# Performance work log

Hardware: AMD Instinct MI355X
Metric: run time of the kernel (lower is better)

Reference implementation:

```python
import jax, jax.numpy as jnp
import numpy as np

jax.config.update("jax_enable_x64", True)

N = 16          # particles per jet
B = 32          # number of jets
L2 = 1e-4       # qpth_l2_strength ('L2' form: Q = L2*I, p = flattened distance matrix)
ITERS = 20      # fixed interior-point iterations (converges well past solver tolerance)
SIGMA = 0.1     # centering parameter


def _build_G(n):
    # Inequality matrix, same layout as the torch code: G = [-I ; marginal-row-sums ; marginal-col-sums]
    m = n * n
    G1 = -np.eye(m)
    G2 = np.zeros((2 * n, m))
    for i in range(n):
        G2[i, i * n:(i + 1) * n] = 1.0      # sum_j x_{ij} <= w1_i
    for j in range(n):
        G2[n + j, j::n] = 1.0               # sum_i x_{ij} <= w2_j
    return jnp.asarray(np.concatenate([G1, G2], axis=0))  # [m + 2n, m]


def _solve_qp(p, h, b, G):
    """Batched infeasible-start primal-dual interior point solver for
    min 0.5*L2*||x||^2 + p.x  s.t.  G x <= h,  1.x = b  (same QP qpth solves)."""
    Bn, m = p.shape
    nin = G.shape[0]
    ones_m = jnp.ones((m,), p.dtype)
    x = jnp.zeros((Bn, m), p.dtype)
    s = jnp.ones((Bn, nin), p.dtype)
    z = jnp.ones((Bn, nin), p.dtype)
    y = jnp.zeros((Bn,), p.dtype)
    eye_m = jnp.eye(m, dtype=p.dtype)

    def step(carry, _):
        x, s, z, y = carry
        mu = jnp.mean(s * z, axis=1)                    # [B]
        rx = L2 * x + p + z @ G + y[:, None]            # dual residual   (A^T y = y * 1)
        rp = x @ G.T + s - h                            # primal ineq residual
        ra = x.sum(1) - b                               # primal eq residual
        rs = s * z - SIGMA * mu[:, None]                # complementarity residual
        d = z / s
        # H = Q + G^T diag(d) G  -> [B, m, m]
        H = L2 * eye_m + jnp.einsum('rk,br,rl->bkl', G, d, G)
        r1 = rx + ((z * rp - rs) / s) @ G
        Lc = jnp.linalg.cholesky(H)

        def chosolve(rhs):  # rhs [B, m] -> H^{-1} rhs
            t = jax.scipy.linalg.solve_triangular(Lc, rhs[..., None], lower=True)
            return jax.scipy.linalg.solve_triangular(Lc, t, lower=True, trans='T')[..., 0]

        u = chosolve(r1)
        v = chosolve(jnp.broadcast_to(ones_m, (Bn, m)))
        dy = (ra - u.sum(1)) / v.sum(1)                 # Schur complement on the 1-row equality
        dx = -u - v * dy[:, None]
        ds = -rp - dx @ G.T
        dz = (-rs - z * ds) / s
        # fraction-to-boundary step
        ds_safe = jnp.where(ds < 0, ds, -jnp.ones_like(ds))
        dz_safe = jnp.where(dz < 0, dz, -jnp.ones_like(dz))
        a_s = jnp.min(jnp.where(ds < 0, -s / ds_safe, jnp.inf), axis=1)
        a_z = jnp.min(jnp.where(dz < 0, -z / dz_safe, jnp.inf), axis=1)
        alpha = 0.99 * jnp.minimum(1.0, jnp.minimum(a_s, a_z))[:, None]
        x = x + alpha * dx
        s = s + alpha * ds
        z = z + alpha * dz
        y = y + alpha[:, 0] * dy
        return (x, s, z, y), None

    (x, s, z, y), _ = jax.lax.scan(step, (x, s, z, y), None, length=ITERS)
    return x


def setup_inputs() -> dict:
    key = jax.random.key(0)
    k1, k2 = jax.random.split(key)
    jets1 = jax.random.uniform(k1, (B, N, 3), dtype=jnp.float32)
    jets2 = jax.random.uniform(k2, (B, N, 3), dtype=jnp.float32)
    return {"jets1": jets1, "jets2": jets2}


def reference(jets1, jets2):
    j1 = jets1.astype(jnp.float64)
    j2 = jets2.astype(jnp.float64)
    nb, n = j1.shape[0], j1.shape[1]
    # pairwise (eta, phi) distances, same sign/epsilon as the torch code
    diffs = -(j1[:, :, None, :2] - j2[:, None, :, :2]) + 1e-12   # [B, n, n, 2]
    dists = jnp.sqrt(jnp.sum(diffs * diffs, axis=3))             # [B, n, n]
    w1 = j1[:, :, 2]
    w2 = j2[:, :, 2]
    p = dists.reshape(nb, n * n)
    h = jnp.concatenate([jnp.zeros((nb, n * n), p.dtype), w1, w2], axis=1)
    b = jnp.minimum(w1.sum(1), w2.sum(1))
    G = _build_G(n)
    flow = _solve_qp(p, h, b, G)                                  # [B, n*n]
    energy_diff = jnp.abs(w1.sum(1) - w2.sum(1))
    emds = jnp.sum(p * flow, axis=1) + energy_diff                # [B]
    return emds
```

## Files before the change

kernel.cpp:

```cpp
#include <hip/hip_runtime.h>
#include <math.h>

#define L2C  1e-4
#define SIGC 0.1
#define NITER 20

#if defined(__has_builtin)
#  if __has_builtin(__builtin_amdgcn_permlane16_swap) && __has_builtin(__builtin_amdgcn_permlane32_swap)
#    define HAVE_PLSWAP 1
#  endif
#  if __has_builtin(__builtin_amdgcn_rcp)
#    define HAVE_RCP64 1
#  endif
#endif
#ifndef HAVE_PLSWAP
#  define HAVE_PLSWAP 0
#endif
#ifndef HAVE_RCP64
#  define HAVE_RCP64 0
#endif

__device__ __forceinline__ double rld(double v, int lane) {
    union { double d; int i[2]; } u, r; u.d = v;
    r.i[0] = __builtin_amdgcn_readlane(u.i[0], lane);
    r.i[1] = __builtin_amdgcn_readlane(u.i[1], lane);
    return r.d;
}
template <int CTRL>
__device__ __forceinline__ double dppd(double v) {
    union { double d; int i[2]; } u, r; u.d = v;
    r.i[0] = __builtin_amdgcn_update_dpp(0, u.i[0], CTRL, 0xF, 0xF, true);
    r.i[1] = __builtin_amdgcn_update_dpp(0, u.i[1], CTRL, 0xF, 0xF, true);
    return r.d;
}
__device__ __forceinline__ double sum16d(double v) {
    v += dppd<0xB1>(v); v += dppd<0x4E>(v); v += dppd<0x124>(v); v += dppd<0x128>(v);
    return v;
}
template <int CTRL>
__device__ __forceinline__ float dppf(float v) {
    return __int_as_float(__builtin_amdgcn_update_dpp(0, __float_as_int(v), CTRL, 0xF, 0xF, true));
}
__device__ __forceinline__ float min16f(float v) {
    v = fminf(v, dppf<0xB1>(v)); v = fminf(v, dppf<0x4E>(v));
    v = fminf(v, dppf<0x124>(v)); v = fminf(v, dppf<0x128>(v));
    return v;
}
__device__ __forceinline__ double mkd(unsigned lo, unsigned hi) {
    union { unsigned u[2]; double d; } r; r.u[0] = lo; r.u[1] = hi; return r.d;
}
__device__ __forceinline__ void dsplit(double v, unsigned &lo, unsigned &hi) {
    union { double d; unsigned u[2]; } x; x.d = v; lo = x.u[0]; hi = x.u[1];
}
__device__ __forceinline__ double cross4d(double v) {
#if HAVE_PLSWAP
    unsigned lo, hi; dsplit(v, lo, hi);
    auto rl = __builtin_amdgcn_permlane16_swap(lo, lo, false, false);
    auto rh = __builtin_amdgcn_permlane16_swap(hi, hi, false, false);
    v = mkd(rl[0], rh[0]) + mkd(rl[1], rh[1]);
    dsplit(v, lo, hi);
    auto sl = __builtin_amdgcn_permlane32_swap(lo, lo, false, false);
    auto sh = __builtin_amdgcn_permlane32_swap(hi, hi, false, false);
    return mkd(sl[0], sh[0]) + mkd(sl[1], sh[1]);
#else
    v += __shfl_xor(v, 16, 64); v += __shfl_xor(v, 32, 64); return v;
#endif
}
__device__ __forceinline__ float cross4minf(float v) {
#if HAVE_PLSWAP
    auto a = __builtin_amdgcn_permlane16_swap(__float_as_uint(v), __float_as_uint(v), false, false);
    v = fminf(__uint_as_float(a[0]), __uint_as_float(a[1]));
    auto b = __builtin_amdgcn_permlane32_swap(__float_as_uint(v), __float_as_uint(v), false, false);
    return fminf(__uint_as_float(b[0]), __uint_as_float(b[1]));
#else
    v = fminf(v, __shfl_xor(v, 16, 64)); v = fminf(v, __shfl_xor(v, 32, 64)); return v;
#endif
}
__device__ __forceinline__ double drcp(double d) {
#if HAVE_RCP64
    double x = __builtin_amdgcn_rcp(d);
#else
    double x = (double)__builtin_amdgcn_rcpf((float)d);
#endif
    x = x * (2.0 - d * x);
    return x;
}
__device__ __forceinline__ float frcpf(float x) { return __builtin_amdgcn_rcpf(x); }

__global__ __launch_bounds__(64, 1) void emd_ip_kernel(const float* __restrict__ jets1,
                                                       const float* __restrict__ jets2,
                                                       float* __restrict__ out) {
    const int l = threadIdx.x;
    const int b = blockIdx.x;
    const int q = l & 15;
    const int r = l >> 4;

    __shared__ double invDl[16 * 17];
    __shared__ double Sst[16 * 17];
    __shared__ double Lst[16 * 17];
    __shared__ double GstR[16], GstI[16];

    const float* p1 = jets1 + b * 48;
    const float* p2 = jets2 + b * 48;

    double ax = (double)p1[3 * q], ay = (double)p1[3 * q + 1];
    double px[4];
#pragma unroll
    for (int c = 0; c < 4; c++) {
        int j = 4 * c + r;
        double d0 = ((double)p2[3 * j]     - ax) + 1e-12;
        double d1 = ((double)p2[3 * j + 1] - ay) + 1e-12;
        px[c] = sqrt(d0 * d0 + d1 * d1);
    }
    double h_rt = (double)p1[3 * q + 2];
    double h_ct[4];
#pragma unroll
    for (int c = 0; c < 4; c++) h_ct[c] = (double)p2[3 * (4 * c + r) + 2];

    double sw1 = sum16d(h_rt);
    double sw2 = sum16d((double)p2[3 * q + 2]);
    const double sB = fmin(sw1, sw2);
    const double sE = fabs(sw1 - sw2);

    double x[4] = {0, 0, 0, 0}, s[4] = {1, 1, 1, 1}, z[4] = {1, 1, 1, 1};
    double yv = 0.0;
    double s_rt = 1.0, z_rt = 1.0;
    double s_ct[4] = {1, 1, 1, 1}, z_ct[4] = {1, 1, 1, 1};
    double rsx = 0.0;
    double cs[4] = {0, 0, 0, 0};
    double ra = -sB;

    for (int it = 0; it < NITER; ++it) {
        double is_rt = drcp(s_rt);
        double iz_rt = drcp(z_rt);
        double srz   = s_rt * iz_rt;
        double is_ct[4], iz_ct[4];
#pragma unroll
        for (int c = 0; c < 4; c++) { is_ct[c] = drcp(s_ct[c]); iz_ct[c] = drcp(z_ct[c]); }
        double is_[4], iD[4];
#pragma unroll
        for (int c = 0; c < 4; c++) {
            is_[c] = drcp(s[c]);
            iD[c] = drcp(L2C + z[c] * is_[c]);
            invDl[q * 17 + 4 * c + r] = iD[c];
        }

        double mub = s[0]*z[0] + s[1]*z[1] + s[2]*z[2] + s[3]*z[3]
                   + 0.25 * (s_rt * z_rt)
                   + 0.0625 * (s_ct[0]*z_ct[0] + s_ct[1]*z_ct[1] + s_ct[2]*z_ct[2] + s_ct[3]*z_ct[3]);
        double mu = sum16d(cross4d(mub)) * (1.0 / 288.0);
        if (!(mu >= 1e-4)) break;
        double sgmu = SIGC * mu;

        double rp_rt = rsx + s_rt - h_rt;
        double rs_rt = s_rt * z_rt - sgmu;
        double tt_rt = (z_rt * (rsx - h_rt) + sgmu) * is_rt;
        double rp_ct[4], rs_ct[4], tt_ct[4];
#pragma unroll
        for (int c = 0; c < 4; c++) {
            rp_ct[c] = cs[c] + s_ct[c] - h_ct[c];
            rs_ct[c] = s_ct[c] * z_ct[c] - sgmu;
            tt_ct[c] = (z_ct[c] * (cs[c] - h_ct[c]) + sgmu) * is_ct[c];
        }

        double rp[4], rs[4], r1[4], rD1[4];
#pragma unroll
        for (int c = 0; c < 4; c++) {
            double rx = L2C * x[c] + px[c] + (-z[c] + z_rt + z_ct[c]) + yv;
            rp[c] = s[c] - x[c];
            rs[c] = s[c] * z[c] - sgmu;
            double tk = (sgmu - z[c] * x[c]) * is_[c];
            r1[c] = rx - tk + tt_rt + tt_ct[c];
            rD1[c] = r1[c] * iD[c];
        }

        double rsI = cross4d(iD[0] + iD[1] + iD[2] + iD[3]);
        double rsR = cross4d(rD1[0] + rD1[1] + rD1[2] + rD1[3]);
        double csI[4], csR[4];
#pragma unroll
        for (int c = 0; c < 4; c++) { csI[c] = sum16d(iD[c]); csR[c] = sum16d(rD1[c]); }

        double ar = drcp(srz + rsI);
        double aR = ar * rsR;
        double aI = ar * rsI;

        double gpR[4], gpI[4], bb[4];
#pragma unroll
        for (int c = 0; c < 4; c++) {
            gpR[c] = csR[c] - sum16d(aR * iD[c]);
            gpI[c] = csI[c] - sum16d(aI * iD[c]);
            bb[c]  = s_ct[c] * iz_ct[c] + csI[c];
            if (q == 4 * c + r) { GstR[q] = gpR[c]; GstI[q] = gpI[c]; }
        }

        double accA[4] = {0, 0, 0, 0}, accB[4] = {0, 0, 0, 0};
#pragma unroll
        for (int t = 0; t < 8; t++) {
            double wA = rld(ar, t) * invDl[t * 17 + q];
            double wB = rld(ar, t + 8) * invDl[(t + 8) * 17 + q];
#pragma unroll
            for (int c = 0; c < 4; c++) {
                accA[c] += wA * invDl[t * 17 + 4 * c + r];
                accB[c] += wB * invDl[(t + 8) * 17 + 4 * c + r];
            }
        }
#pragma unroll
        for (int c = 0; c < 4; c++)
            Sst[q * 17 + 4 * c + r] = ((q == 4 * c + r) ? bb[c] : 0.0) - (accA[c] + accB[c]);

        double Sr[16];
#pragma unroll
        for (int j2 = 0; j2 < 16; j2++) Sr[j2] = Sst[q * 17 + j2];

        double flo[16];
#pragma unroll
        for (int kk = 0; kk < 16; kk++)
            flo[kk] = fmax(1e-12 * fabs(rld(Sr[kk], kk)), 1e-280);

        double invdv = 0.0;
        double pcand = 0.0;
#pragma unroll
        for (int kk = 0; kk < 16; kk++) {
            double praw = (kk == 0) ? rld(Sr[0], 0) : rld(pcand, kk);
            double dkk = fmax(praw, flo[kk]);
            double inv = drcp(dkk);
            invdv = (q == kk) ? inv : invdv;
            double Lc = Sr[kk] * inv;
            if (l < 16) Lst[kk * 17 + l] = Lc;
            if (kk < 15) pcand = Sr[kk + 1] - Sr[kk] * Lc;
#pragma unroll
            for (int jj = kk + 1; jj < 16; jj++)
                Sr[jj] -= Sr[kk] * rld(Lc, jj);
            Sr[kk] = Lc;
        }

        double y1 = GstR[q], y2 = GstI[q];
        double LTr[16];
#pragma unroll
        for (int kk = 0; kk < 16; kk++) LTr[kk] = Lst[q * 17 + kk];

#pragma unroll
        for (int kk = 0; kk < 16; kk++) {
            double t1 = rld(y1, kk);
            double t2 = rld(y2, kk);
            if (q > kk) { y1 -= Sr[kk] * t1; y2 -= Sr[kk] * t2; }
        }
        y1 *= invdv;
        y2 *= invdv;
#pragma unroll
        for (int kk = 15; kk >= 0; kk--) {
            double t1 = rld(y1, kk);
            double t2 = rld(y2, kk);
            if (q < kk) { y1 -= LTr[kk] * t1; y2 -= LTr[kk] * t2; }
        }

        double qc1c[4], qcvc[4];
#pragma unroll
        for (int c = 0; c < 4; c++) {
            qc1c[c] = __shfl(y1, 4 * c + r, 64);
            qcvc[c] = __shfl(y2, 4 * c + r, 64);
        }

        double pr1 = iD[0]*qc1c[0] + iD[1]*qc1c[1] + iD[2]*qc1c[2] + iD[3]*qc1c[3];
        double prv = iD[0]*qcvc[0] + iD[1]*qcvc[1] + iD[2]*qcvc[2] + iD[3]*qcvc[3];
        double qr1 = ar * (rsR - cross4d(pr1));
        double qrv = ar * (rsI - cross4d(prv));

        double u[4], v[4];
#pragma unroll
        for (int c = 0; c < 4; c++) {
            u[c] = (r1[c] - qr1 - qc1c[c]) * iD[c];
            v[c] = (1.0  - qrv - qcvc[c]) * iD[c];
        }
        double usum = sum16d(cross4d(u[0] + u[1] + u[2] + u[3]));
        double vsum = sum16d(cross4d(v[0] + v[1] + v[2] + v[3]));
        double dy = (ra - usum) * drcp(vsum);

        double dx[4];
#pragma unroll
        for (int c = 0; c < 4; c++) dx[c] = -u[c] - v[c] * dy;
        double rsdx = cross4d(dx[0] + dx[1] + dx[2] + dx[3]);
        double csdx[4];
#pragma unroll
        for (int c = 0; c < 4; c++) csdx[c] = sum16d(dx[c]);
        double sumdx = -usum - vsum * dy;

        float amP = 1e30f, amD = 1e30f;
        double ds[4], dz[4];
#pragma unroll
        for (int c = 0; c < 4; c++) {
            ds[c] = dx[c] - rp[c];
            dz[c] = -(rs[c] + z[c] * ds[c]) * is_[c];
            if (ds[c] < 0.0) amP = fminf(amP, (float)s[c] * frcpf((float)(-ds[c])));
            if (dz[c] < 0.0) amD = fminf(amD, (float)z[c] * frcpf((float)(-dz[c])));
        }
        double ds_rt = -rp_rt - rsdx;
        double dz_rt = -(rs_rt + z_rt * ds_rt) * is_rt;
        if (ds_rt < 0.0) amP = fminf(amP, (float)s_rt * frcpf((float)(-ds_rt)));
        if (dz_rt < 0.0) amD = fminf(amD, (float)z_rt * frcpf((float)(-dz_rt)));
        double ds_ct[4], dz_ct[4];
#pragma unroll
        for (int c = 0; c < 4; c++) {
            ds_ct[c] = -rp_ct[c] - csdx[c];
            dz_ct[c] = -(rs_ct[c] + z_ct[c] * ds_ct[c]) * is_ct[c];
            if (ds_ct[c] < 0.0) amP = fminf(amP, (float)s_ct[c] * frcpf((float)(-ds_ct[c])));
            if (dz_ct[c] < 0.0) amD = fminf(amD, (float)z_ct[c] * frcpf((float)(-dz_ct[c])));
        }
        float aPf = min16f(cross4minf(amP));
        float aDf = min16f(cross4minf(amD));
        double alphaP = 0.99 * fmin(1.0, (double)aPf);
        double alphaD = 0.99 * fmin(1.0, (double)aDf);
        bool good = ((dy - dy) == 0.0);
        alphaP = good ? alphaP : 0.0;
        alphaD = good ? alphaD : 0.0;

#pragma unroll
        for (int c = 0; c < 4; c++) {
            x[c] += alphaP * dx[c];
            s[c] += alphaP * ds[c];
            z[c] += alphaD * dz[c];
            s_ct[c] += alphaP * ds_ct[c];
            z_ct[c] += alphaD * dz_ct[c];
            cs[c] += alphaP * csdx[c];
        }
        yv += alphaD * dy;
        s_rt += alphaP * ds_rt;
        z_rt += alphaD * dz_rt;
        rsx += alphaP * rsdx;
        ra  += alphaP * sumdx;
    }

    double e = sum16d(cross4d(px[0]*x[0] + px[1]*x[1] + px[2]*x[2] + px[3]*x[3]));
    if (l == 0) out[b] = (float)(e + sE);
}

extern "C" void kernel_launch(void* const* d_in, const int* in_sizes, int n_in,
                              void* d_out, int out_size, void* d_ws, size_t ws_size,
                              hipStream_t stream) {
    const float* jets1 = (const float*)d_in[0];
    const float* jets2 = (const float*)d_in[1];
    float* out = (float*)d_out;
    int B = in_sizes[0] / 48;
    emd_ip_kernel<<<dim3(B), dim3(64), 0, stream>>>(jets1, jets2, out);
}
```

Measured before the change: 113.0 us.

## Share reciprocals, fuse forward solve into Cholesky, transpose Schur matrix via permlane swaps

Each pair of reciprocals, such as 1/s and 1/z, is now computed from a single reciprocal of their product. The Schur matrix is transposed with permlane16/32 swaps instead of a round trip through LDS, guarded by a runtime check of the swap semantics. The two right-hand sides are packed into one register split across half-waves, and the forward substitution is folded into the Cholesky factorization loop. A few reductions are merged, and rsdx is derived algebraically. Together these cut readlane, LDS and reciprocal work on the serial per-iteration critical path, at some risk to rounding behaviour and to correctness of the permlane assumptions.

```diff
diff --git a/kernel.cpp b/kernel.cpp
--- a/kernel.cpp
+++ b/kernel.cpp
@@ -98,7 +98,7 @@
     __shared__ double invDl[16 * 17];
     __shared__ double Sst[16 * 17];
     __shared__ double Lst[16 * 17];
-    __shared__ double GstR[16], GstI[16];
+    __shared__ double Gst[2][16];
 
     const float* p1 = jets1 + b * 48;
     const float* p2 = jets2 + b * 48;
@@ -122,6 +122,17 @@
     const double sB = fmin(sw1, sw2);
     const double sE = fabs(sw1 - sw2);
 
+#if HAVE_PLSWAP
+    auto pr16 = __builtin_amdgcn_permlane16_swap((unsigned)l, (unsigned)l, false, false);
+    auto pr32 = __builtin_amdgcn_permlane32_swap((unsigned)l, (unsigned)l, false, false);
+    const bool convOK = (__builtin_amdgcn_readfirstlane((int)pr16[0]) == 0) &&
+                        (__builtin_amdgcn_readfirstlane((int)pr16[1]) == 16) &&
+                        (__builtin_amdgcn_readfirstlane((int)pr32[0]) == 0) &&
+                        (__builtin_amdgcn_readfirstlane((int)pr32[1]) == 32);
+#else
+    const bool convOK = false;
+#endif
+
     double x[4] = {0, 0, 0, 0}, s[4] = {1, 1, 1, 1}, z[4] = {1, 1, 1, 1};
     double yv = 0.0;
     double s_rt = 1.0, z_rt = 1.0;
@@ -131,35 +142,44 @@
     double ra = -sB;
 
     for (int it = 0; it < NITER; ++it) {
-        double is_rt = drcp(s_rt);
-        double iz_rt = drcp(z_rt);
-        double srz   = s_rt * iz_rt;
-        double is_ct[4], iz_ct[4];
-#pragma unroll
-        for (int c = 0; c < 4; c++) { is_ct[c] = drcp(s_ct[c]); iz_ct[c] = drcp(z_ct[c]); }
-        double is_[4], iD[4];
-#pragma unroll
-        for (int c = 0; c < 4; c++) {
-            is_[c] = drcp(s[c]);
-            iD[c] = drcp(L2C + z[c] * is_[c]);
+        double prt = s_rt * z_rt;
+        double irt = drcp(prt);
+        double is_rt = z_rt * irt, iz_rt = s_rt * irt;
+        double srz = (s_rt * s_rt) * irt;
+        double pct[4], is_ct[4], iz_ct[4];
+#pragma unroll
+        for (int c = 0; c < 4; c++) {
+            pct[c] = s_ct[c] * z_ct[c];
+            double ict = drcp(pct[c]);
+            is_ct[c] = z_ct[c] * ict;
+            iz_ct[c] = s_ct[c] * ict;
+        }
+        double szc[4], is_[4], iD[4];
+#pragma unroll
+        for (int c = 0; c < 4; c++) {
+            szc[c] = s[c] * z[c];
+            double tc = fma(L2C, s[c], z[c]);
+            double ip = drcp(s[c] * tc);
+            is_[c] = tc * ip;
+            iD[c]  = (s[c] * s[c]) * ip;
             invDl[q * 17 + 4 * c + r] = iD[c];
         }
 
-        double mub = s[0]*z[0] + s[1]*z[1] + s[2]*z[2] + s[3]*z[3]
-                   + 0.25 * (s_rt * z_rt)
-                   + 0.0625 * (s_ct[0]*z_ct[0] + s_ct[1]*z_ct[1] + s_ct[2]*z_ct[2] + s_ct[3]*z_ct[3]);
+        double mub = szc[0] + szc[1] + szc[2] + szc[3]
+                   + 0.25 * prt
+                   + 0.0625 * (pct[0] + pct[1] + pct[2] + pct[3]);
         double mu = sum16d(cross4d(mub)) * (1.0 / 288.0);
         if (!(mu >= 1e-4)) break;
         double sgmu = SIGC * mu;
 
         double rp_rt = rsx + s_rt - h_rt;
-        double rs_rt = s_rt * z_rt - sgmu;
+        double rs_rt = prt - sgmu;
         double tt_rt = (z_rt * (rsx - h_rt) + sgmu) * is_rt;
         double rp_ct[4], rs_ct[4], tt_ct[4];
 #pragma unroll
         for (int c = 0; c < 4; c++) {
             rp_ct[c] = cs[c] + s_ct[c] - h_ct[c];
-            rs_ct[c] = s_ct[c] * z_ct[c] - sgmu;
+            rs_ct[c] = pct[c] - sgmu;
             tt_ct[c] = (z_ct[c] * (cs[c] - h_ct[c]) + sgmu) * is_ct[c];
         }
 
@@ -168,7 +188,7 @@
         for (int c = 0; c < 4; c++) {
             double rx = L2C * x[c] + px[c] + (-z[c] + z_rt + z_ct[c]) + yv;
             rp[c] = s[c] - x[c];
-            rs[c] = s[c] * z[c] - sgmu;
+            rs[c] = szc[c] - sgmu;
             double tk = (sgmu - z[c] * x[c]) * is_[c];
             r1[c] = rx - tk + tt_rt + tt_ct[c];
             rD1[c] = r1[c] * iD[c];
@@ -176,21 +196,21 @@
 
         double rsI = cross4d(iD[0] + iD[1] + iD[2] + iD[3]);
         double rsR = cross4d(rD1[0] + rD1[1] + rD1[2] + rD1[3]);
-        double csI[4], csR[4];
-#pragma unroll
-        for (int c = 0; c < 4; c++) { csI[c] = sum16d(iD[c]); csR[c] = sum16d(rD1[c]); }
+        double csI[4];
+#pragma unroll
+        for (int c = 0; c < 4; c++) csI[c] = sum16d(iD[c]);
 
         double ar = drcp(srz + rsI);
         double aR = ar * rsR;
         double aI = ar * rsI;
 
-        double gpR[4], gpI[4], bb[4];
-#pragma unroll
-        for (int c = 0; c < 4; c++) {
-            gpR[c] = csR[c] - sum16d(aR * iD[c]);
-            gpI[c] = csI[c] - sum16d(aI * iD[c]);
-            bb[c]  = s_ct[c] * iz_ct[c] + csI[c];
-            if (q == 4 * c + r) { GstR[q] = gpR[c]; GstI[q] = gpI[c]; }
+        double bb[4];
+#pragma unroll
+        for (int c = 0; c < 4; c++) {
+            double gpR = sum16d(rD1[c] - aR * iD[c]);
+            double gpI = csI[c] - sum16d(aI * iD[c]);
+            bb[c] = s_ct[c] * iz_ct[c] + csI[c];
+            if (q == 4 * c + r) { Gst[0][q] = gpR; Gst[1][q] = gpI; }
         }
 
         double accA[4] = {0, 0, 0, 0}, accB[4] = {0, 0, 0, 0};
@@ -204,18 +224,43 @@
                 accB[c] += wB * invDl[(t + 8) * 17 + 4 * c + r];
             }
         }
+        double Sv[4];
 #pragma unroll
         for (int c = 0; c < 4; c++)
-            Sst[q * 17 + 4 * c + r] = ((q == 4 * c + r) ? bb[c] : 0.0) - (accA[c] + accB[c]);
+            Sv[c] = ((q == 4 * c + r) ? bb[c] : 0.0) - (accA[c] + accB[c]);
 
         double Sr[16];
-#pragma unroll
-        for (int j2 = 0; j2 < 16; j2++) Sr[j2] = Sst[q * 17 + j2];
+#if HAVE_PLSWAP
+        if (convOK) {
+#pragma unroll
+            for (int c = 0; c < 4; c++) {
+                unsigned xl, xh; dsplit(Sv[c], xl, xh);
+                auto sl = __builtin_amdgcn_permlane16_swap(xl, xl, false, false);
+                auto sh = __builtin_amdgcn_permlane16_swap(xh, xh, false, false);
+                auto e = __builtin_amdgcn_permlane32_swap(sl[0], sl[0], false, false);
+                auto f = __builtin_amdgcn_permlane32_swap(sh[0], sh[0], false, false);
+                auto g = __builtin_amdgcn_permlane32_swap(sl[1], sl[1], false, false);
+                auto h = __builtin_amdgcn_permlane32_swap(sh[1], sh[1], false, false);
+                Sr[4 * c + 0] = mkd(e[0], f[0]);
+                Sr[4 * c + 2] = mkd(e[1], f[1]);
+                Sr[4 * c + 1] = mkd(g[0], h[0]);
+                Sr[4 * c + 3] = mkd(g[1], h[1]);
+            }
+        } else
+#endif
+        {
+#pragma unroll
+            for (int c = 0; c < 4; c++) Sst[q * 17 + 4 * c + r] = Sv[c];
+#pragma unroll
+            for (int j2 = 0; j2 < 16; j2++) Sr[j2] = Sst[q * 17 + j2];
+        }
 
         double flo[16];
 #pragma unroll
         for (int kk = 0; kk < 16; kk++)
             flo[kk] = fmax(1e-12 * fabs(rld(Sr[kk], kk)), 1e-280);
+
+        double ysol = Gst[r >> 1][q];
 
         double invdv = 0.0;
         double pcand = 0.0;
@@ -228,37 +273,35 @@
             double Lc = Sr[kk] * inv;
             if (l < 16) Lst[kk * 17 + l] = Lc;
             if (kk < 15) pcand = Sr[kk + 1] - Sr[kk] * Lc;
+            double t1 = rld(ysol, kk);
+            double t2 = rld(ysol, kk + 32);
+            double tt = (r < 2) ? t1 : t2;
+            if (q > kk) ysol -= Lc * tt;
 #pragma unroll
             for (int jj = kk + 1; jj < 16; jj++)
                 Sr[jj] -= Sr[kk] * rld(Lc, jj);
             Sr[kk] = Lc;
         }
 
-        double y1 = GstR[q], y2 = GstI[q];
+        ysol *= invdv;
+
         double LTr[16];
 #pragma unroll
         for (int kk = 0; kk < 16; kk++) LTr[kk] = Lst[q * 17 + kk];
 
 #pragma unroll
-        for (int kk = 0; kk < 16; kk++) {
-            double t1 = rld(y1, kk);
-            double t2 = rld(y2, kk);
-            if (q > kk) { y1 -= Sr[kk] * t1; y2 -= Sr[kk] * t2; }
-        }
-        y1 *= invdv;
-        y2 *= invdv;
-#pragma unroll
         for (int kk = 15; kk >= 0; kk--) {
-            double t1 = rld(y1, kk);
-            double t2 = rld(y2, kk);
-            if (q < kk) { y1 -= LTr[kk] * t1; y2 -= LTr[kk] * t2; }
+            double t1 = rld(ysol, kk);
+            double t2 = rld(ysol, kk + 32);
+            double tt = (r < 2) ? t1 : t2;
+            if (q < kk) ysol -= LTr[kk] * tt;
         }
 
         double qc1c[4], qcvc[4];
 #pragma unroll
         for (int c = 0; c < 4; c++) {
-            qc1c[c] = __shfl(y1, 4 * c + r, 64);
-            qcvc[c] = __shfl(y2, 4 * c + r, 64);
+            qc1c[c] = __shfl(ysol, 4 * c + r, 64);
+            qcvc[c] = __shfl(ysol, 32 + 4 * c + r, 64);
         }
 
         double pr1 = iD[0]*qc1c[0] + iD[1]*qc1c[1] + iD[2]*qc1c[2] + iD[3]*qc1c[3];
@@ -272,14 +315,16 @@
             u[c] = (r1[c] - qr1 - qc1c[c]) * iD[c];
             v[c] = (1.0  - qrv - qcvc[c]) * iD[c];
         }
-        double usum = sum16d(cross4d(u[0] + u[1] + u[2] + u[3]));
-        double vsum = sum16d(cross4d(v[0] + v[1] + v[2] + v[3]));
+        double urow = cross4d(u[0] + u[1] + u[2] + u[3]);
+        double vrow = cross4d(v[0] + v[1] + v[2] + v[3]);
+        double usum = sum16d(urow);
+        double vsum = sum16d(vrow);
         double dy = (ra - usum) * drcp(vsum);
 
         double dx[4];
 #pragma unroll
         for (int c = 0; c < 4; c++) dx[c] = -u[c] - v[c] * dy;
-        double rsdx = cross4d(dx[0] + dx[1] + dx[2] + dx[3]);
+        double rsdx = -urow - vrow * dy;
         double csdx[4];
 #pragma unroll
         for (int c = 0; c < 4; c++) csdx[c] = sum16d(dx[c]);
```

Measured after the change: 112.6 us. About the same (-0.3%).
